# Optimization experiments

Measured on AMD Instinct MI355X. Metric: run time of the kernel, lower is better.

Reference implementation:

```python
import jax, jax.numpy as jnp
import numpy as np

D = 1024

def setup_inputs() -> dict:
    key = jax.random.key(0)
    k1, k2, k3, k4 = jax.random.split(key, 4)
    context = jax.random.normal(k1, (32, 2048, D), dtype=jnp.float32)
    # nn.Linear(dim, dim, bias=False): weight [D, D], applied as x @ W.T
    W = jax.random.normal(k2, (D, D), dtype=jnp.float32) / np.sqrt(D)
    # nn.Linear(dim, 1): weight [1, D], bias [1]
    v = jax.random.normal(k3, (D,), dtype=jnp.float32) / np.sqrt(D)
    b = jax.random.normal(k4, (), dtype=jnp.float32) * 0.01
    return {"context": context, "W": W, "v": v, "b": b}

def reference(context, W, v, b):
    # context: [B, S, D]
    h = jnp.tanh(jnp.einsum('bsd,ed->bse', context, W))      # [B, S, D]
    attn_logits = jnp.einsum('bsd,d->bs', h, v) + b          # [B, S]
    attn = jax.nn.softmax(attn_logits, axis=-1)              # softmax over sourceL
    weighted_context = jnp.einsum('bs,bsd->bd', attn, context)
    return weighted_context, attn
```

## Files before the change

### kernel.cpp

```cpp
#include <hip/hip_runtime.h>
#include <stdint.h>

#define BDIM 32
#define SDIM 2048
#define DDIM 1024
#define MDIM (BDIM * SDIM)

typedef __bf16 bf16x8 __attribute__((ext_vector_type(8)));
typedef float  f32x4  __attribute__((ext_vector_type(4)));


__device__ inline unsigned short f2bf(float f) {
  union { float f; unsigned u; } un; un.f = f;
  unsigned r = un.u + 0x7fffu + ((un.u >> 16) & 1u);
  return (unsigned short)(r >> 16);
}

__device__ inline float fast_tanh(float x) {
  float e = __expf(2.0f * x);
  return 1.0f - 2.0f / (e + 1.0f);
}

__device__ inline void gl_lds16(const unsigned short* g, unsigned short* l) {
  __builtin_amdgcn_global_load_lds(
      (__attribute__((address_space(1))) unsigned int*)(void*)(uintptr_t)g,
      (__attribute__((address_space(3))) unsigned int*)l,
      16, 0, 0);
}


__global__ __launch_bounds__(256) void cvt_kernel(const float* __restrict__ src,
                                                  unsigned short* __restrict__ dst) {
  size_t i = (size_t)blockIdx.x * 256 + threadIdx.x;
  const float4* s4 = (const float4*)src;
  float4 a = s4[2 * i];
  float4 b = s4[2 * i + 1];
  uint4 o;
  o.x = (unsigned)f2bf(a.x) | ((unsigned)f2bf(a.y) << 16);
  o.y = (unsigned)f2bf(a.z) | ((unsigned)f2bf(a.w) << 16);
  o.z = (unsigned)f2bf(b.x) | ((unsigned)f2bf(b.y) << 16);
  o.w = (unsigned)f2bf(b.z) | ((unsigned)f2bf(b.w) << 16);
  ((uint4*)dst)[i] = o;
}


__global__ __launch_bounds__(256) void gemm_logits(
    const unsigned short* __restrict__ A,
    const unsigned short* __restrict__ Bw,
    const float* __restrict__ v,
    float* __restrict__ logits)
{
  __shared__ __align__(16) unsigned short Al[128 * 64];
  __shared__ __align__(16) unsigned short Wl[128 * 64];

  const int t  = threadIdx.x;
  const int l  = (blockIdx.x & 7) * 512 + (blockIdx.x >> 3);
  const int mt = l >> 3;
  const int nt = l & 7;
  const int m0 = mt * 128;
  const int n0 = nt * 128;
  const int w    = t >> 6;
  const int lane = t & 63;
  const int c = lane & 15;
  const int q = lane >> 4;
  const int wm = (w >> 1) * 64;
  const int wn = (w & 1) * 64;

  float vv[4];
#pragma unroll
  for (int ni = 0; ni < 4; ++ni) vv[ni] = v[n0 + wn + ni * 16 + c];

  f32x4 acc[4][4] = {};

  const int rt  = t >> 3;
  const int sA  = t & 7;
  const int psl = sA ^ (rt & 7);
  const unsigned short* ga = A  + (size_t)(m0 + rt) * DDIM + psl * 8;
  const unsigned short* gb = Bw + (size_t)(n0 + rt) * DDIM + psl * 8;
  unsigned short* lab = Al + (size_t)(t & 192) * 8;
  unsigned short* lwb = Wl + (size_t)(t & 192) * 8;

  for (int kt = 0; kt < 16; ++kt) {
    const int k0 = kt * 64;
#pragma unroll
    for (int r = 0; r < 4; ++r)
      gl_lds16(ga + (size_t)(r * 32) * DDIM + k0, lab + r * 2048);
#pragma unroll
    for (int r = 0; r < 4; ++r)
      gl_lds16(gb + (size_t)(r * 32) * DDIM + k0, lwb + r * 2048);
    __syncthreads();

#pragma unroll
    for (int kk = 0; kk < 2; ++kk) {
      bf16x8 af[4], bfr[4];
      const int slot = ((kk * 4 + q) ^ (c & 7)) * 8;
#pragma unroll
      for (int mi = 0; mi < 4; ++mi)
        af[mi] = *(const bf16x8*)&Al[(wm + mi * 16 + c) * 64 + slot];
#pragma unroll
      for (int ni = 0; ni < 4; ++ni)
        bfr[ni] = *(const bf16x8*)&Wl[(wn + ni * 16 + c) * 64 + slot];
#pragma unroll
      for (int mi = 0; mi < 4; ++mi)
#pragma unroll
        for (int ni = 0; ni < 4; ++ni)
          acc[mi][ni] = __builtin_amdgcn_mfma_f32_16x16x32_bf16(
              af[mi], bfr[ni], acc[mi][ni], 0, 0, 0);
    }
    __syncthreads();
  }

#pragma unroll
  for (int mi = 0; mi < 4; ++mi) {
    float p0 = 0.f, p1 = 0.f, p2 = 0.f, p3 = 0.f;
#pragma unroll
    for (int ni = 0; ni < 4; ++ni) {
      const float vvn = vv[ni];
      p0 += fast_tanh(acc[mi][ni][0]) * vvn;
      p1 += fast_tanh(acc[mi][ni][1]) * vvn;
      p2 += fast_tanh(acc[mi][ni][2]) * vvn;
      p3 += fast_tanh(acc[mi][ni][3]) * vvn;
    }
#pragma unroll
    for (int mask = 1; mask <= 8; mask <<= 1) {
      p0 += __shfl_xor(p0, mask);
      p1 += __shfl_xor(p1, mask);
      p2 += __shfl_xor(p2, mask);
      p3 += __shfl_xor(p3, mask);
    }
    if (c == 0) {
      float* lp = logits + (m0 + wm + mi * 16 + q * 4);
      atomicAdd(lp + 0, p0);
      atomicAdd(lp + 1, p1);
      atomicAdd(lp + 2, p2);
      atomicAdd(lp + 3, p3);
    }
  }
}


__global__ __launch_bounds__(256) void softmax_kernel(float* __restrict__ la) {
  const int b = blockIdx.x;
  const int t = threadIdx.x;
  float* p = la + (size_t)b * SDIM;
  float x[8];
#pragma unroll
  for (int i = 0; i < 8; ++i) x[i] = p[i * 256 + t];
  float m = x[0];
#pragma unroll
  for (int i = 1; i < 8; ++i) m = fmaxf(m, x[i]);
#pragma unroll
  for (int mask = 1; mask < 64; mask <<= 1) m = fmaxf(m, __shfl_xor(m, mask));
  __shared__ float redm[4], reds[4];
  const int w = t >> 6, lane = t & 63;
  if (lane == 0) redm[w] = m;
  __syncthreads();
  m = fmaxf(fmaxf(redm[0], redm[1]), fmaxf(redm[2], redm[3]));
  float e[8];
  float s = 0.f;
#pragma unroll
  for (int i = 0; i < 8; ++i) { e[i] = __expf(x[i] - m); s += e[i]; }
#pragma unroll
  for (int mask = 1; mask < 64; mask <<= 1) s += __shfl_xor(s, mask);
  if (lane == 0) reds[w] = s;
  __syncthreads();
  s = reds[0] + reds[1] + reds[2] + reds[3];
  const float inv = 1.0f / s;
#pragma unroll
  for (int i = 0; i < 8; ++i) p[i * 256 + t] = e[i] * inv;
}


__global__ __launch_bounds__(256) void wsum_part(const float* __restrict__ ctx,
                                                 const float* __restrict__ attn,
                                                 float* __restrict__ part) {
  const int b  = blockIdx.x >> 6;
  const int sc = blockIdx.x & 63;
  const int t  = threadIdx.x;
  const float* cp = ctx + ((size_t)b * SDIM + sc * 32) * DDIM + t * 4;
  const float* ap = attn + (size_t)b * SDIM + sc * 32;
  float4 acc = {0.f, 0.f, 0.f, 0.f};
#pragma unroll 4
  for (int s = 0; s < 32; ++s) {
    const float a = ap[s];
    const float4 cv = *(const float4*)(cp + (size_t)s * DDIM);
    acc.x += a * cv.x; acc.y += a * cv.y; acc.z += a * cv.z; acc.w += a * cv.w;
  }
  *(float4*)(part + (size_t)blockIdx.x * DDIM + t * 4) = acc;
}


__global__ __launch_bounds__(256) void wsum_reduce(const float* __restrict__ part,
                                                   float* __restrict__ wc) {
  const int b = blockIdx.x >> 2;
  const int d = (blockIdx.x & 3) * 256 + threadIdx.x;
  float s = 0.f;
#pragma unroll
  for (int sc = 0; sc < 64; ++sc)
    s += part[((size_t)b * 64 + sc) * DDIM + d];
  wc[(size_t)b * DDIM + d] = s;
}


extern "C" void kernel_launch(void* const* d_in, const int* in_sizes, int n_in,
                              void* d_out, int out_size, void* d_ws, size_t ws_size,
                              hipStream_t stream) {
  const float* ctx = (const float*)d_in[0];
  const float* W   = (const float*)d_in[1];
  const float* v   = (const float*)d_in[2];

  float* out_wc   = (float*)d_out;
  float* out_attn = out_wc + BDIM * DDIM;

  unsigned short* W_bf   = (unsigned short*)d_ws;
  unsigned short* ctx_bf = W_bf + (size_t)DDIM * DDIM;
  float* part = (float*)(void*)ctx_bf;

  hipMemsetAsync(out_attn, 0, (size_t)BDIM * SDIM * sizeof(float), stream);

  cvt_kernel<<<(DDIM * DDIM) / (256 * 8), 256, 0, stream>>>(W, W_bf);
  cvt_kernel<<<(MDIM * DDIM) / (256 * 8), 256, 0, stream>>>(ctx, ctx_bf);
  gemm_logits<<<(MDIM / 128) * (DDIM / 128), 256, 0, stream>>>(ctx_bf, W_bf, v, out_attn);
  softmax_kernel<<<BDIM, 256, 0, stream>>>(out_attn);
  wsum_part<<<BDIM * 64, 256, 0, stream>>>(ctx, out_attn, part);
  wsum_reduce<<<(BDIM * DDIM) / 256, 256, 0, stream>>>(part, out_wc);
}
```

Baseline: 626.9 us.

## Fuse ctx bf16 conversion into GEMM and replace logit atomics with partial planes

```diff
diff --git a/kernel.cpp b/kernel.cpp
--- a/kernel.cpp
+++ b/kernel.cpp
@@ -45,10 +45,10 @@
 
 
 __global__ __launch_bounds__(256) void gemm_logits(
-    const unsigned short* __restrict__ A,
+    const float* __restrict__ ctx,
     const unsigned short* __restrict__ Bw,
     const float* __restrict__ v,
-    float* __restrict__ logits)
+    float* __restrict__ logitsP)
 {
   __shared__ __align__(16) unsigned short Al[128 * 64];
   __shared__ __align__(16) unsigned short Wl[128 * 64];
@@ -75,19 +75,28 @@
   const int rt  = t >> 3;
   const int sA  = t & 7;
   const int psl = sA ^ (rt & 7);
-  const unsigned short* ga = A  + (size_t)(m0 + rt) * DDIM + psl * 8;
+  const float* gA = ctx + (size_t)(m0 + rt) * DDIM + sA * 8;
   const unsigned short* gb = Bw + (size_t)(n0 + rt) * DDIM + psl * 8;
-  unsigned short* lab = Al + (size_t)(t & 192) * 8;
   unsigned short* lwb = Wl + (size_t)(t & 192) * 8;
 
   for (int kt = 0; kt < 16; ++kt) {
     const int k0 = kt * 64;
 #pragma unroll
     for (int r = 0; r < 4; ++r)
-      gl_lds16(ga + (size_t)(r * 32) * DDIM + k0, lab + r * 2048);
-#pragma unroll
-    for (int r = 0; r < 4; ++r)
       gl_lds16(gb + (size_t)(r * 32) * DDIM + k0, lwb + r * 2048);
+#pragma unroll
+    for (int j = 0; j < 4; ++j) {
+      const int row = j * 32 + rt;
+      const float* g = gA + (size_t)(j * 32) * DDIM + k0;
+      float4 a = *(const float4*)g;
+      float4 b = *(const float4*)(g + 4);
+      bf16x8 cv;
+      cv[0] = (__bf16)a.x; cv[1] = (__bf16)a.y;
+      cv[2] = (__bf16)a.z; cv[3] = (__bf16)a.w;
+      cv[4] = (__bf16)b.x; cv[5] = (__bf16)b.y;
+      cv[6] = (__bf16)b.z; cv[7] = (__bf16)b.w;
+      *(bf16x8*)&Al[row * 64 + psl * 8] = cv;
+    }
     __syncthreads();
 
 #pragma unroll
@@ -110,6 +119,7 @@
     __syncthreads();
   }
 
+  const size_t plane = (size_t)(nt * 2 + (w & 1)) * MDIM;
 #pragma unroll
   for (int mi = 0; mi < 4; ++mi) {
     float p0 = 0.f, p1 = 0.f, p2 = 0.f, p3 = 0.f;
@@ -129,23 +139,26 @@
       p3 += __shfl_xor(p3, mask);
     }
     if (c == 0) {
-      float* lp = logits + (m0 + wm + mi * 16 + q * 4);
-      atomicAdd(lp + 0, p0);
-      atomicAdd(lp + 1, p1);
-      atomicAdd(lp + 2, p2);
-      atomicAdd(lp + 3, p3);
-    }
-  }
-}
-
-
-__global__ __launch_bounds__(256) void softmax_kernel(float* __restrict__ la) {
+      float4 o = {p0, p1, p2, p3};
+      *(float4*)(logitsP + plane + m0 + wm + mi * 16 + q * 4) = o;
+    }
+  }
+}
+
+
+__global__ __launch_bounds__(256) void softmax_kernel(const float* __restrict__ P,
+                                                      float* __restrict__ attn) {
   const int b = blockIdx.x;
   const int t = threadIdx.x;
-  float* p = la + (size_t)b * SDIM;
   float x[8];
 #pragma unroll
-  for (int i = 0; i < 8; ++i) x[i] = p[i * 256 + t];
+  for (int i = 0; i < 8; ++i) {
+    const size_t off = (size_t)b * SDIM + i * 256 + t;
+    float s = 0.f;
+#pragma unroll
+    for (int pl = 0; pl < 16; ++pl) s += P[(size_t)pl * MDIM + off];
+    x[i] = s;
+  }
   float m = x[0];
 #pragma unroll
   for (int i = 1; i < 8; ++i) m = fmaxf(m, x[i]);
@@ -166,6 +179,7 @@
   __syncthreads();
   s = reds[0] + reds[1] + reds[2] + reds[3];
   const float inv = 1.0f / s;
+  float* p = attn + (size_t)b * SDIM;
 #pragma unroll
   for (int i = 0; i < 8; ++i) p[i * 256 + t] = e[i] * inv;
 }
@@ -212,16 +226,13 @@
   float* out_wc   = (float*)d_out;
   float* out_attn = out_wc + BDIM * DDIM;
 
-  unsigned short* W_bf   = (unsigned short*)d_ws;
-  unsigned short* ctx_bf = W_bf + (size_t)DDIM * DDIM;
-  float* part = (float*)(void*)ctx_bf;
-
-  hipMemsetAsync(out_attn, 0, (size_t)BDIM * SDIM * sizeof(float), stream);
+  float* logitsP = (float*)d_ws;
+  float* part    = logitsP + (size_t)16 * MDIM;
+  unsigned short* W_bf = (unsigned short*)(part + (size_t)2048 * DDIM);
 
   cvt_kernel<<<(DDIM * DDIM) / (256 * 8), 256, 0, stream>>>(W, W_bf);
-  cvt_kernel<<<(MDIM * DDIM) / (256 * 8), 256, 0, stream>>>(ctx, ctx_bf);
-  gemm_logits<<<(MDIM / 128) * (DDIM / 128), 256, 0, stream>>>(ctx_bf, W_bf, v, out_attn);
-  softmax_kernel<<<BDIM, 256, 0, stream>>>(out_attn);
+  gemm_logits<<<(MDIM / 128) * (DDIM / 128), 256, 0, stream>>>(ctx, W_bf, v, logitsP);
+  softmax_kernel<<<BDIM, 256, 0, stream>>>(logitsP, out_attn);
   wsum_part<<<BDIM * 64, 256, 0, stream>>>(ctx, out_attn, part);
   wsum_reduce<<<(BDIM * DDIM) / 256, 256, 0, stream>>>(part, out_wc);
 }
```

Result: faster. 557.0 us (-11.1%).
